# Kernel optimization log

Measured on AMD Instinct MI355X. Metric: run time of the kernel, lower is better.

## Reference

```python
import jax, jax.numpy as jnp
import numpy as np

# Inner model dims (concrete MLP standing in for the wrapped keras model)
D_IN, HID, D_OUT = 1024, 2048, 10
POP, STD = 40, 0.1
S1 = D_IN * HID          # end of W1
S2 = S1 + HID            # end of b1
S3 = S2 + HID * D_OUT    # end of W2
N_PARAMS = S3 + D_OUT    # 2,119,690


def _flatten_weights(W1, b1, W2, b2):
    # tf.concat([reshape(w, [-1]) for w in trainable_weights])
    return jnp.concatenate([W1.reshape(-1), b1, W2.reshape(-1), b2])


def _mse_loss(flat_w, x, y):
    # expand_flat_trainable_weights + forward + compiled_loss (MSE)
    W1 = flat_w[:S1].reshape(D_IN, HID)
    b1 = flat_w[S1:S2]
    W2 = flat_w[S2:S3].reshape(HID, D_OUT)
    b2 = flat_w[S3:]
    pred = jax.nn.relu(x @ W1 + b1) @ W2 + b2
    return jnp.mean((pred - y) ** 2)


def _centered_ranks(t):
    # compute_centered_ranks: argsort-based ranks in [0, n), centered to [-0.5, 0.5]
    flat = t.reshape(-1)
    n = flat.shape[0]
    ranks = jnp.zeros((n,), jnp.float32).at[jnp.argsort(flat)].set(
        jnp.arange(n, dtype=jnp.float32))
    return (ranks / (n - 1) - 0.5).reshape(t.shape)


def setup_inputs() -> dict:
    key = jax.random.key(0)
    ks = jax.random.split(key, 5)
    return {
        "x": jax.random.normal(ks[0], (256, D_IN), jnp.float32),
        "y": jax.random.normal(ks[1], (256, D_OUT), jnp.float32),
        "W1": jax.random.normal(ks[2], (D_IN, HID), jnp.float32) * 0.02,
        "b1": jnp.zeros((HID,), jnp.float32),
        "W2": jax.random.normal(ks[3], (HID, D_OUT), jnp.float32) * 0.02,
        "b2": jnp.zeros((D_OUT,), jnp.float32),
        "noise": jax.random.normal(ks[4], (POP, N_PARAMS), jnp.float32),
    }


def reference(x, y, W1, b1, W2, b2, noise):
    flat_w = _flatten_weights(W1, b1, W2, b2)          # [N]
    eps = noise * STD                                   # stddev-scaled noise [POP, N]
    # parity: i even -> +1, i odd -> -1 (antithetic pairs)
    parity = jnp.array([1.0, -1.0], jnp.float32)
    perturbed = flat_w[None, None, :] + eps[:, None, :] * parity[None, :, None]  # [POP,2,N]
    # batched replacement for the pop_size*2 sequential forward passes
    losses = jax.vmap(jax.vmap(lambda w: _mse_loss(w, x, y)))(perturbed)  # [POP, 2]
    proc = _centered_ranks(losses)
    proc = proc[:, 0] - proc[:, 1]                      # [POP]
    grad = jnp.tensordot(eps, proc, axes=[[0], [0]]) / (POP * STD)  # [N]
    return grad
```

## Files before the change

### kernel.cpp

```cpp
#include <hip/hip_runtime.h>


#define NPLL 2119690LL
#define S1_  2097152
#define S2_  2099200
#define S3_  2119680

#define WS_PP   524288
#define WS_LOSS 3801088
#define WS_G    3801168

typedef _Float16 f16;
typedef __fp16   fp16x2 __attribute__((ext_vector_type(2)));
typedef _Float16 f16x8 __attribute__((ext_vector_type(8)));
typedef float    f32x4 __attribute__((ext_vector_type(4)));

__device__ __forceinline__ unsigned pk2r(float a, float b, float& ra, float& rb) {
  fp16x2 h = __builtin_amdgcn_cvt_pkrtz(a, b);
  ra = a - (float)h[0];
  rb = b - (float)h[1];
  return __builtin_bit_cast(unsigned, h);
}
__device__ __forceinline__ unsigned pk2(float a, float b) {
  fp16x2 h = __builtin_amdgcn_cvt_pkrtz(a, b);
  return __builtin_bit_cast(unsigned, h);
}

__global__ __launch_bounds__(256) void k_base(const float* __restrict__ x,
                                              const float* __restrict__ W1,
                                              const float* __restrict__ b1,
                                              float* __restrict__ base) {
  constexpr int STR = 72;
  __shared__ float xs[32 * STR];
  __shared__ float es[32 * STR];
  const int t  = threadIdx.x;
  const int j0 = blockIdx.x * 64;
  const int b0 = blockIdx.y * 32;
  const int tj = t & 15;
  const int tb = t >> 4;
  float acc[4][2] = {};
  for (int k0 = 0; k0 < 1024; k0 += 32) {
    __syncthreads();
    {
      int bb = t >> 3, kq = t & 7;
      float4 v = *(const float4*)&x[(size_t)(b0 + bb) * 1024 + k0 + kq * 4];
      int kb = kq * 4;
      xs[(kb + 0) * STR + bb] = v.x;
      xs[(kb + 1) * STR + bb] = v.y;
      xs[(kb + 2) * STR + bb] = v.z;
      xs[(kb + 3) * STR + bb] = v.w;
    }
#pragma unroll
    for (int r = 0; r < 2; ++r) {
      int idx = t + r * 256;
      int k = idx >> 4, jq = idx & 15, col = jq * 4;
      float4 v = *(const float4*)&W1[(size_t)(k0 + k) * 2048 + j0 + col];
      *(float4*)&es[k * STR + col + 4 * (col >> 5)] = v;
    }
    __syncthreads();
#pragma unroll 8
    for (int k = 0; k < 32; ++k) {
      const int ce = tj * 4;
      float4 e = *(const float4*)&es[k * STR + ce + 4 * (ce >> 5)];
      float2 a = *(const float2*)&xs[k * STR + tb * 2];
      acc[0][0] += e.x * a.x; acc[0][1] += e.x * a.y;
      acc[1][0] += e.y * a.x; acc[1][1] += e.y * a.y;
      acc[2][0] += e.z * a.x; acc[2][1] += e.z * a.y;
      acc[3][0] += e.w * a.x; acc[3][1] += e.w * a.y;
    }
  }
#pragma unroll
  for (int jj = 0; jj < 4; ++jj) {
    int j = j0 + tj * 4 + jj;
    float bv = b1[j];
    float2 o = make_float2(acc[jj][0] + bv, acc[jj][1] + bv);
    *(float2*)&base[(size_t)j * 256 + b0 + tb * 2] = o;
  }
}

#define ESTR 72
__global__ __launch_bounds__(256, 2) void k_big(const float* __restrict__ x,
                                                const float* __restrict__ noise,
                                                const float* __restrict__ W2,
                                                const float* __restrict__ base,
                                                float* __restrict__ pp) {
  __shared__ __align__(16) f16 eA[128 * ESTR];
  __shared__ __align__(16) f16 xB[128 * ESTR];
  __shared__ float w2l[1280], e2l[1280], e1l[128];
  __shared__ float red[1280];

  const int t    = threadIdx.x;
  const int p    = blockIdx.x >> 1, bt = blockIdx.x & 1, jt = blockIdx.y;
  const int j0   = jt * 128, b0 = bt * 128;
  const int wave = t >> 6, lane = t & 63;
  const int lm   = lane & 15, g8 = (lane >> 4) * 8;
  const int g4   = (lane >> 4) * 4;
  const int wj0  = (wave & 1) * 64, wb0 = (wave >> 1) * 64;
  const size_t pN = (size_t)p * NPLL;
  const int rl = t & 63;
  const int kq = (t >> 6) * 8;

  for (int i = t; i < 1280; i += 256) {
    w2l[i] = W2[j0 * 10 + i];
    e2l[i] = noise[pN + S2_ + (size_t)j0 * 10 + i];
  }
  if (t < 128) e1l[t] = noise[pN + S1_ + j0 + t];

  float vE0[8], vE1[8], vX0[8], vX1[8];
  f32x4 acc[4][4];
#pragma unroll
  for (int a = 0; a < 4; ++a)
#pragma unroll
    for (int b = 0; b < 4; ++b) acc[a][b] = (f32x4){0.f, 0.f, 0.f, 0.f};

#define LOADK(K0)                                                              \
  do {                                                                         \
    const float* eg = &noise[pN + (size_t)((K0) + kq) * 2048 + j0 + rl];       \
    _Pragma("unroll") for (int d = 0; d < 8; ++d) {                            \
      vE0[d] = eg[(size_t)d * 2048];                                           \
      vE1[d] = eg[(size_t)d * 2048 + 64];                                      \
    }                                                                          \
    const float* xg = &x[(size_t)(b0 + rl) * 1024 + (K0) + kq];                \
    float4 a0 = *(const float4*)xg;                                            \
    float4 a1 = *(const float4*)(xg + 4);                                      \
    float4 c0 = *(const float4*)(xg + 65536);                                  \
    float4 c1 = *(const float4*)(xg + 65540);                                  \
    vX0[0] = a0.x; vX0[1] = a0.y; vX0[2] = a0.z; vX0[3] = a0.w;                \
    vX0[4] = a1.x; vX0[5] = a1.y; vX0[6] = a1.z; vX0[7] = a1.w;                \
    vX1[0] = c0.x; vX1[1] = c0.y; vX1[2] = c0.z; vX1[3] = c0.w;                \
    vX1[4] = c1.x; vX1[5] = c1.y; vX1[6] = c1.z; vX1[7] = c1.w;                \
  } while (0)

#define CVW(V, DST)                                                            \
  do {                                                                         \
    float r0, r1, r2, r3, r4, r5, r6, r7;                                      \
    uint4 H, L;                                                                \
    H.x = pk2r(V[0], V[1], r0, r1);                                            \
    H.y = pk2r(V[2], V[3], r2, r3);                                            \
    H.z = pk2r(V[4], V[5], r4, r5);                                            \
    H.w = pk2r(V[6], V[7], r6, r7);                                            \
    *(uint4*)(DST) = H;                                                        \
    L.x = pk2(r0, r1); L.y = pk2(r2, r3);                                      \
    L.z = pk2(r4, r5); L.w = pk2(r6, r7);                                      \
    *(uint4*)((DST) + 32) = L;                                                 \
  } while (0)

  LOADK(0);
  for (int ks = 0; ks < 32; ++ks) {
    __syncthreads();
    CVW(vE0, &eA[rl * ESTR + kq]);
    CVW(vE1, &eA[(rl + 64) * ESTR + kq]);
    CVW(vX0, &xB[rl * ESTR + kq]);
    CVW(vX1, &xB[(rl + 64) * ESTR + kq]);
    if (ks < 31) LOADK((ks + 1) * 32);
    __syncthreads();
    f16x8 Ah[4], Al[4], Bh[4], Bl[4];
#pragma unroll
    for (int mf = 0; mf < 4; ++mf) {
      Ah[mf] = *(const f16x8*)&eA[(wj0 + mf * 16 + lm) * ESTR + g8];
      Al[mf] = *(const f16x8*)&eA[(wj0 + mf * 16 + lm) * ESTR + 32 + g8];
      Bh[mf] = *(const f16x8*)&xB[(wb0 + mf * 16 + lm) * ESTR + g8];
      Bl[mf] = *(const f16x8*)&xB[(wb0 + mf * 16 + lm) * ESTR + 32 + g8];
    }
#pragma unroll
    for (int mf = 0; mf < 4; ++mf)
#pragma unroll
      for (int nf = 0; nf < 4; ++nf) {
        acc[mf][nf] = __builtin_amdgcn_mfma_f32_16x16x32_f16(Ah[mf], Bh[nf], acc[mf][nf], 0, 0, 0);
        acc[mf][nf] = __builtin_amdgcn_mfma_f32_16x16x32_f16(Ah[mf], Bl[nf], acc[mf][nf], 0, 0, 0);
        acc[mf][nf] = __builtin_amdgcn_mfma_f32_16x16x32_f16(Al[mf], Bh[nf], acc[mf][nf], 0, 0, 0);
      }
  }

  float ppvP[4][10] = {};
  float ppvM[4][10] = {};
#pragma unroll
  for (int mf = 0; mf < 4; ++mf)
#pragma unroll
    for (int r = 0; r < 4; ++r) {
      const int jl = wj0 + mf * 16 + g4 + r;
      const float e1v = e1l[jl];
      float w2p[10], w2m[10];
#pragma unroll
      for (int o = 0; o < 10; ++o) {
        float w2 = w2l[jl * 10 + o], e2 = e2l[jl * 10 + o];
        w2p[o] = fmaf(0.1f, e2, w2);
        w2m[o] = fmaf(-0.1f, e2, w2);
      }
#pragma unroll
      for (int nf = 0; nf < 4; ++nf) {
        const int bl = wb0 + nf * 16 + lm;
        const float bs = base[(size_t)(j0 + jl) * 256 + b0 + bl];
        const float tv = acc[mf][nf][r] + e1v;
        const float hp = fmaxf(fmaf(0.1f, tv, bs), 0.f);
        const float hm = fmaxf(fmaf(-0.1f, tv, bs), 0.f);
#pragma unroll
        for (int o = 0; o < 10; ++o) {
          ppvP[nf][o] = fmaf(hp, w2p[o], ppvP[nf][o]);
          ppvM[nf][o] = fmaf(hm, w2m[o], ppvM[nf][o]);
        }
      }
    }

#pragma unroll
  for (int nf = 0; nf < 4; ++nf)
#pragma unroll
    for (int o = 0; o < 10; ++o) {
      float v = ppvP[nf][o];
      v += __shfl_xor(v, 16, 64);
      v += __shfl_xor(v, 32, 64);
      ppvP[nf][o] = v;
      float u = ppvM[nf][o];
      u += __shfl_xor(u, 16, 64);
      u += __shfl_xor(u, 32, 64);
      ppvM[nf][o] = u;
    }

  const int wjh = wave & 1, wbh = wave >> 1;
  __syncthreads();
  if (wjh == 1 && lane < 16) {
#pragma unroll
    for (int nf = 0; nf < 4; ++nf)
#pragma unroll
      for (int o = 0; o < 10; ++o)
        red[(wbh * 64 + nf * 16 + lane) * 10 + o] = ppvP[nf][o];
  }
  __syncthreads();
  if (wjh == 0 && lane < 16) {
#pragma unroll
    for (int nf = 0; nf < 4; ++nf) {
      const int bl = wbh * 64 + nf * 16 + lane;
#pragma unroll
      for (int o = 0; o < 10; ++o)
        pp[((((size_t)p * 2 + 0) * 16 + jt) * 256 + b0 + bl) * 10 + o] =
            ppvP[nf][o] + red[bl * 10 + o];
    }
  }
  __syncthreads();
  if (wjh == 1 && lane < 16) {
#pragma unroll
    for (int nf = 0; nf < 4; ++nf)
#pragma unroll
      for (int o = 0; o < 10; ++o)
        red[(wbh * 64 + nf * 16 + lane) * 10 + o] = ppvM[nf][o];
  }
  __syncthreads();
  if (wjh == 0 && lane < 16) {
#pragma unroll
    for (int nf = 0; nf < 4; ++nf) {
      const int bl = wbh * 64 + nf * 16 + lane;
#pragma unroll
      for (int o = 0; o < 10; ++o)
        pp[((((size_t)p * 2 + 1) * 16 + jt) * 256 + b0 + bl) * 10 + o] =
            ppvM[nf][o] + red[bl * 10 + o];
    }
  }
#undef LOADK
#undef CVW
}

__global__ __launch_bounds__(256) void k_loss(const float* __restrict__ pp,
                                              const float* __restrict__ y,
                                              const float* __restrict__ b2,
                                              const float* __restrict__ noise,
                                              float* __restrict__ loss) {
  const int b = threadIdx.x;
  const int p = blockIdx.x >> 1, s = blockIdx.x & 1;
  const float sf = s ? -0.1f : 0.1f;
  const size_t pN = (size_t)p * NPLL;
  float pred[10];
#pragma unroll
  for (int o = 0; o < 10; ++o) pred[o] = b2[o] + sf * noise[pN + S3_ + o];
  for (int jt = 0; jt < 16; ++jt) {
    const float* src = &pp[((((size_t)p * 2 + s) * 16 + jt) * 256 + b) * 10];
#pragma unroll
    for (int o = 0; o < 10; ++o) pred[o] += src[o];
  }
  float e = 0.f;
#pragma unroll
  for (int o = 0; o < 10; ++o) {
    float d = pred[o] - y[b * 10 + o];
    e += d * d;
  }
  __shared__ float red[256];
  red[b] = e;
  __syncthreads();
  for (int st = 128; st > 0; st >>= 1) {
    if (b < st) red[b] += red[b + st];
    __syncthreads();
  }
  if (b == 0) loss[blockIdx.x] = red[0] * (1.0f / 2560.0f);
}

__global__ void k_rank(const float* __restrict__ loss, float* __restrict__ g) {
  __shared__ float ls[80];
  __shared__ float rk[80];
  const int t = threadIdx.x;
  if (t < 80) ls[t] = loss[t];
  __syncthreads();
  if (t < 80) {
    float li = ls[t];
    int r = 0;
    for (int j = 0; j < 80; ++j) {
      float lj = ls[j];
      r += (lj < li) || (lj == li && j < t);
    }
    rk[t] = (float)r;
  }
  __syncthreads();
  if (t < 40) g[t] = (rk[2 * t] - rk[2 * t + 1]) * (1.0f / (79.0f * 40.0f));
}

__global__ __launch_bounds__(256) void k_grad(const float* __restrict__ noise,
                                              const float* __restrict__ g,
                                              float* __restrict__ out) {
  __shared__ float gg[40];
  const int t = threadIdx.x;
  if (t < 40) gg[t] = g[t];
  __syncthreads();
  const long long NH = NPLL / 2;
  long long idx = (long long)blockIdx.x * 256 + t;
  if (idx >= NH) return;
  float2 a = make_float2(0.f, 0.f);
#pragma unroll 8
  for (int p = 0; p < 40; ++p) {
    float2 v = *(const float2*)&noise[(size_t)p * NPLL + idx * 2];
    a.x += v.x * gg[p];
    a.y += v.y * gg[p];
  }
  *(float2*)&out[idx * 2] = a;
}

extern "C" void kernel_launch(void* const* d_in, const int* in_sizes, int n_in,
                              void* d_out, int out_size, void* d_ws, size_t ws_size,
                              hipStream_t stream) {
  const float* x     = (const float*)d_in[0];
  const float* y     = (const float*)d_in[1];
  const float* W1    = (const float*)d_in[2];
  const float* b1    = (const float*)d_in[3];
  const float* W2    = (const float*)d_in[4];
  const float* b2    = (const float*)d_in[5];
  const float* noise = (const float*)d_in[6];
  float* out  = (float*)d_out;
  float* ws   = (float*)d_ws;
  float* base = ws;
  float* pp   = ws + WS_PP;
  float* loss = ws + WS_LOSS;
  float* g    = ws + WS_G;

  k_base<<<dim3(32, 8), 256, 0, stream>>>(x, W1, b1, base);
  k_big<<<dim3(80, 16), 256, 0, stream>>>(x, noise, W2, base, pp);
  k_loss<<<80, 256, 0, stream>>>(pp, y, b2, noise, loss);
  k_rank<<<1, 128, 0, stream>>>(loss, g);
  k_grad<<<4141, 256, 0, stream>>>(noise, g, out);
}
```

Before: 390.7 us.

## Retile big kernel over full batch, presplit x to fp16 hi/lo, store fp16 partials

Each k_big block now covers 64 hidden units across all 256 batch rows instead of 128x128, so each noise element is loaded once rather than twice. A new kernel splits x into fp16 hi/lo halves up front, and k_big reads those directly from global memory, dropping the per-block conversion and the LDS staging of x. The epilogue loops over the two signs to cut register pressure. Per-tile partial predictions are stored as packed fp16, which lowers traffic but adds rounding error to the losses and could change their ranking.

```diff
diff --git a/kernel.cpp b/kernel.cpp
--- a/kernel.cpp
+++ b/kernel.cpp
@@ -9,6 +9,8 @@
 #define WS_PP   524288
 #define WS_LOSS 3801088
 #define WS_G    3801168
+#define WS_XH   3801216
+#define WS_XL   3932288
 
 typedef _Float16 f16;
 typedef __fp16   fp16x2 __attribute__((ext_vector_type(2)));
@@ -24,6 +26,11 @@
 __device__ __forceinline__ unsigned pk2(float a, float b) {
   fp16x2 h = __builtin_amdgcn_cvt_pkrtz(a, b);
   return __builtin_bit_cast(unsigned, h);
+}
+__device__ __forceinline__ unsigned packh(float a, float b) {
+  union { f16 h[2]; unsigned u; } v;
+  v.h[0] = (f16)a; v.h[1] = (f16)b;
+  return v.u;
 }
 
 __global__ __launch_bounds__(256) void k_base(const float* __restrict__ x,
@@ -78,89 +85,94 @@
   }
 }
 
+__global__ __launch_bounds__(256) void k_xsplit(const float* __restrict__ x,
+                                                f16* __restrict__ xh,
+                                                f16* __restrict__ xl) {
+  const int i = (blockIdx.x * 256 + threadIdx.x) * 8;
+  float4 a = *(const float4*)&x[i];
+  float4 b = *(const float4*)&x[i + 4];
+  float v[8] = {a.x, a.y, a.z, a.w, b.x, b.y, b.z, b.w};
+  float r[8];
+  uint4 H, L;
+  H.x = pk2r(v[0], v[1], r[0], r[1]);
+  H.y = pk2r(v[2], v[3], r[2], r[3]);
+  H.z = pk2r(v[4], v[5], r[4], r[5]);
+  H.w = pk2r(v[6], v[7], r[6], r[7]);
+  L.x = pk2(r[0], r[1]); L.y = pk2(r[2], r[3]);
+  L.z = pk2(r[4], r[5]); L.w = pk2(r[6], r[7]);
+  *(uint4*)&xh[i] = H;
+  *(uint4*)&xl[i] = L;
+}
+
 #define ESTR 72
-__global__ __launch_bounds__(256, 2) void k_big(const float* __restrict__ x,
+__global__ __launch_bounds__(256, 2) void k_big(const f16* __restrict__ xh,
+                                                const f16* __restrict__ xl,
                                                 const float* __restrict__ noise,
                                                 const float* __restrict__ W2,
                                                 const float* __restrict__ base,
-                                                float* __restrict__ pp) {
-  __shared__ __align__(16) f16 eA[128 * ESTR];
-  __shared__ __align__(16) f16 xB[128 * ESTR];
-  __shared__ float w2l[1280], e2l[1280], e1l[128];
-  __shared__ float red[1280];
+                                                unsigned* __restrict__ ppu) {
+  __shared__ __align__(16) f16 eA[64 * ESTR];
+  __shared__ float w2l[640], e2l[640], e1l[64];
 
   const int t    = threadIdx.x;
-  const int p    = blockIdx.x >> 1, bt = blockIdx.x & 1, jt = blockIdx.y;
-  const int j0   = jt * 128, b0 = bt * 128;
+  const int jt   = blockIdx.x, p = blockIdx.y;
+  const int j0   = jt * 64;
   const int wave = t >> 6, lane = t & 63;
-  const int lm   = lane & 15, g8 = (lane >> 4) * 8;
-  const int g4   = (lane >> 4) * 4;
-  const int wj0  = (wave & 1) * 64, wb0 = (wave >> 1) * 64;
+  const int lm   = lane & 15, g8 = (lane >> 4) * 8, g4 = (lane >> 4) * 4;
+  const int wb   = wave;
   const size_t pN = (size_t)p * NPLL;
-  const int rl = t & 63;
-  const int kq = (t >> 6) * 8;
-
-  for (int i = t; i < 1280; i += 256) {
+  const int rl = lane;
+  const int kq = wave * 8;
+
+  for (int i = t; i < 640; i += 256) {
     w2l[i] = W2[j0 * 10 + i];
     e2l[i] = noise[pN + S2_ + (size_t)j0 * 10 + i];
   }
-  if (t < 128) e1l[t] = noise[pN + S1_ + j0 + t];
-
-  float vE0[8], vE1[8], vX0[8], vX1[8];
+  if (t < 64) e1l[t] = noise[pN + S1_ + j0 + t];
+
+  float ve[8];
   f32x4 acc[4][4];
 #pragma unroll
   for (int a = 0; a < 4; ++a)
 #pragma unroll
     for (int b = 0; b < 4; ++b) acc[a][b] = (f32x4){0.f, 0.f, 0.f, 0.f};
 
-#define LOADK(K0)                                                              \
+#define LOADE(K0)                                                              \
   do {                                                                         \
     const float* eg = &noise[pN + (size_t)((K0) + kq) * 2048 + j0 + rl];       \
-    _Pragma("unroll") for (int d = 0; d < 8; ++d) {                            \
-      vE0[d] = eg[(size_t)d * 2048];                                           \
-      vE1[d] = eg[(size_t)d * 2048 + 64];                                      \
-    }                                                                          \
-    const float* xg = &x[(size_t)(b0 + rl) * 1024 + (K0) + kq];                \
-    float4 a0 = *(const float4*)xg;                                            \
-    float4 a1 = *(const float4*)(xg + 4);                                      \
-    float4 c0 = *(const float4*)(xg + 65536);                                  \
-    float4 c1 = *(const float4*)(xg + 65540);                                  \
-    vX0[0] = a0.x; vX0[1] = a0.y; vX0[2] = a0.z; vX0[3] = a0.w;                \
-    vX0[4] = a1.x; vX0[5] = a1.y; vX0[6] = a1.z; vX0[7] = a1.w;                \
-    vX1[0] = c0.x; vX1[1] = c0.y; vX1[2] = c0.z; vX1[3] = c0.w;                \
-    vX1[4] = c1.x; vX1[5] = c1.y; vX1[6] = c1.z; vX1[7] = c1.w;                \
+    _Pragma("unroll") for (int d = 0; d < 8; ++d) ve[d] = eg[(size_t)d * 2048];\
   } while (0)
 
-#define CVW(V, DST)                                                            \
-  do {                                                                         \
-    float r0, r1, r2, r3, r4, r5, r6, r7;                                      \
-    uint4 H, L;                                                                \
-    H.x = pk2r(V[0], V[1], r0, r1);                                            \
-    H.y = pk2r(V[2], V[3], r2, r3);                                            \
-    H.z = pk2r(V[4], V[5], r4, r5);                                            \
-    H.w = pk2r(V[6], V[7], r6, r7);                                            \
-    *(uint4*)(DST) = H;                                                        \
-    L.x = pk2(r0, r1); L.y = pk2(r2, r3);                                      \
-    L.z = pk2(r4, r5); L.w = pk2(r6, r7);                                      \
-    *(uint4*)((DST) + 32) = L;                                                 \
-  } while (0)
-
-  LOADK(0);
+  LOADE(0);
   for (int ks = 0; ks < 32; ++ks) {
-    __syncthreads();
-    CVW(vE0, &eA[rl * ESTR + kq]);
-    CVW(vE1, &eA[(rl + 64) * ESTR + kq]);
-    CVW(vX0, &xB[rl * ESTR + kq]);
-    CVW(vX1, &xB[(rl + 64) * ESTR + kq]);
-    if (ks < 31) LOADK((ks + 1) * 32);
-    __syncthreads();
-    f16x8 Ah[4], Al[4], Bh[4], Bl[4];
+    const int k0 = ks * 32;
+    __syncthreads();
+    {
+      float r0, r1, r2, r3, r4, r5, r6, r7;
+      uint4 H, L;
+      H.x = pk2r(ve[0], ve[1], r0, r1);
+      H.y = pk2r(ve[2], ve[3], r2, r3);
+      H.z = pk2r(ve[4], ve[5], r4, r5);
+      H.w = pk2r(ve[6], ve[7], r6, r7);
+      *(uint4*)&eA[rl * ESTR + kq] = H;
+      L.x = pk2(r0, r1); L.y = pk2(r2, r3);
+      L.z = pk2(r4, r5); L.w = pk2(r6, r7);
+      *(uint4*)&eA[rl * ESTR + 32 + kq] = L;
+    }
+    f16x8 Bh[4], Bl[4];
+#pragma unroll
+    for (int nf = 0; nf < 4; ++nf) {
+      const size_t bo = (size_t)(wb * 64 + nf * 16 + lm) * 1024 + k0 + g8;
+      Bh[nf] = *(const f16x8*)&xh[bo];
+      Bl[nf] = *(const f16x8*)&xl[bo];
+    }
+    if (ks < 31) LOADE((ks + 1) * 32);
+    __syncthreads();
+    f16x8 Ah[4], Al[4];
 #pragma unroll
     for (int mf = 0; mf < 4; ++mf) {
-      Ah[mf] = *(const f16x8*)&eA[(wj0 + mf * 16 + lm) * ESTR + g8];
-      Al[mf] = *(const f16x8*)&eA[(wj0 + mf * 16 + lm) * ESTR + 32 + g8];
-      Bh[mf] = *(const f16x8*)&xB[(wb0 + mf * 16 + lm) * ESTR + g8];
-      Bl[mf] = *(const f16x8*)&xB[(wb0 + mf * 16 + lm) * ESTR + 32 + g8];
+      Ah[mf] = *(const f16x8*)&eA[(mf * 16 + lm) * ESTR + g8];
+      Al[mf] = *(const f16x8*)&eA[(mf * 16 + lm) * ESTR + 32 + g8];
     }
 #pragma unroll
     for (int mf = 0; mf < 4; ++mf)
@@ -172,94 +184,59 @@
       }
   }
 
-  float ppvP[4][10] = {};
-  float ppvM[4][10] = {};
-#pragma unroll
-  for (int mf = 0; mf < 4; ++mf)
-#pragma unroll
-    for (int r = 0; r < 4; ++r) {
-      const int jl = wj0 + mf * 16 + g4 + r;
-      const float e1v = e1l[jl];
-      float w2p[10], w2m[10];
-#pragma unroll
-      for (int o = 0; o < 10; ++o) {
-        float w2 = w2l[jl * 10 + o], e2 = e2l[jl * 10 + o];
-        w2p[o] = fmaf(0.1f, e2, w2);
-        w2m[o] = fmaf(-0.1f, e2, w2);
-      }
-#pragma unroll
-      for (int nf = 0; nf < 4; ++nf) {
-        const int bl = wb0 + nf * 16 + lm;
-        const float bs = base[(size_t)(j0 + jl) * 256 + b0 + bl];
-        const float tv = acc[mf][nf][r] + e1v;
-        const float hp = fmaxf(fmaf(0.1f, tv, bs), 0.f);
-        const float hm = fmaxf(fmaf(-0.1f, tv, bs), 0.f);
-#pragma unroll
-        for (int o = 0; o < 10; ++o) {
-          ppvP[nf][o] = fmaf(hp, w2p[o], ppvP[nf][o]);
-          ppvM[nf][o] = fmaf(hm, w2m[o], ppvM[nf][o]);
+#pragma unroll 1
+  for (int s = 0; s < 2; ++s) {
+    const float sf = s ? -0.1f : 0.1f;
+    float ppv[4][10];
+#pragma unroll
+    for (int nf = 0; nf < 4; ++nf)
+#pragma unroll
+      for (int o = 0; o < 10; ++o) ppv[nf][o] = 0.f;
+#pragma unroll
+    for (int mf = 0; mf < 4; ++mf)
+#pragma unroll
+      for (int r = 0; r < 4; ++r) {
+        const int jl = mf * 16 + g4 + r;
+        const float e1v = e1l[jl];
+        float w2s[10];
+#pragma unroll
+        for (int o = 0; o < 10; ++o)
+          w2s[o] = fmaf(sf, e2l[jl * 10 + o], w2l[jl * 10 + o]);
+#pragma unroll
+        for (int nf = 0; nf < 4; ++nf) {
+          const int bl = wb * 64 + nf * 16 + lm;
+          const float bs = base[(size_t)(j0 + jl) * 256 + bl];
+          const float h = fmaxf(fmaf(sf, acc[mf][nf][r] + e1v, bs), 0.f);
+#pragma unroll
+          for (int o = 0; o < 10; ++o) ppv[nf][o] = fmaf(h, w2s[o], ppv[nf][o]);
         }
       }
-    }
-
-#pragma unroll
-  for (int nf = 0; nf < 4; ++nf)
-#pragma unroll
-    for (int o = 0; o < 10; ++o) {
-      float v = ppvP[nf][o];
-      v += __shfl_xor(v, 16, 64);
-      v += __shfl_xor(v, 32, 64);
-      ppvP[nf][o] = v;
-      float u = ppvM[nf][o];
-      u += __shfl_xor(u, 16, 64);
-      u += __shfl_xor(u, 32, 64);
-      ppvM[nf][o] = u;
-    }
-
-  const int wjh = wave & 1, wbh = wave >> 1;
-  __syncthreads();
-  if (wjh == 1 && lane < 16) {
 #pragma unroll
     for (int nf = 0; nf < 4; ++nf)
 #pragma unroll
-      for (int o = 0; o < 10; ++o)
-        red[(wbh * 64 + nf * 16 + lane) * 10 + o] = ppvP[nf][o];
-  }
-  __syncthreads();
-  if (wjh == 0 && lane < 16) {
-#pragma unroll
-    for (int nf = 0; nf < 4; ++nf) {
-      const int bl = wbh * 64 + nf * 16 + lane;
-#pragma unroll
-      for (int o = 0; o < 10; ++o)
-        pp[((((size_t)p * 2 + 0) * 16 + jt) * 256 + b0 + bl) * 10 + o] =
-            ppvP[nf][o] + red[bl * 10 + o];
-    }
-  }
-  __syncthreads();
-  if (wjh == 1 && lane < 16) {
-#pragma unroll
-    for (int nf = 0; nf < 4; ++nf)
-#pragma unroll
-      for (int o = 0; o < 10; ++o)
-        red[(wbh * 64 + nf * 16 + lane) * 10 + o] = ppvM[nf][o];
-  }
-  __syncthreads();
-  if (wjh == 0 && lane < 16) {
-#pragma unroll
-    for (int nf = 0; nf < 4; ++nf) {
-      const int bl = wbh * 64 + nf * 16 + lane;
-#pragma unroll
-      for (int o = 0; o < 10; ++o)
-        pp[((((size_t)p * 2 + 1) * 16 + jt) * 256 + b0 + bl) * 10 + o] =
-            ppvM[nf][o] + red[bl * 10 + o];
-    }
-  }
-#undef LOADK
-#undef CVW
-}
-
-__global__ __launch_bounds__(256) void k_loss(const float* __restrict__ pp,
+      for (int o = 0; o < 10; ++o) {
+        float v = ppv[nf][o];
+        v += __shfl_xor(v, 16, 64);
+        v += __shfl_xor(v, 32, 64);
+        ppv[nf][o] = v;
+      }
+    if (lane < 16) {
+#pragma unroll
+      for (int nf = 0; nf < 4; ++nf) {
+        const int bl = wb * 64 + nf * 16 + lm;
+        const size_t u0 = ((((size_t)p * 2 + s) * 32 + jt) * 256 + bl) * 5;
+        ppu[u0 + 0] = packh(ppv[nf][0], ppv[nf][1]);
+        ppu[u0 + 1] = packh(ppv[nf][2], ppv[nf][3]);
+        ppu[u0 + 2] = packh(ppv[nf][4], ppv[nf][5]);
+        ppu[u0 + 3] = packh(ppv[nf][6], ppv[nf][7]);
+        ppu[u0 + 4] = packh(ppv[nf][8], ppv[nf][9]);
+      }
+    }
+  }
+#undef LOADE
+}
+
+__global__ __launch_bounds__(256) void k_loss(const unsigned* __restrict__ ppu,
                                               const float* __restrict__ y,
                                               const float* __restrict__ b2,
                                               const float* __restrict__ noise,
@@ -271,10 +248,15 @@
   float pred[10];
 #pragma unroll
   for (int o = 0; o < 10; ++o) pred[o] = b2[o] + sf * noise[pN + S3_ + o];
-  for (int jt = 0; jt < 16; ++jt) {
-    const float* src = &pp[((((size_t)p * 2 + s) * 16 + jt) * 256 + b) * 10];
-#pragma unroll
-    for (int o = 0; o < 10; ++o) pred[o] += src[o];
+  for (int jt = 0; jt < 32; ++jt) {
+    const size_t u0 = ((((size_t)p * 2 + s) * 32 + jt) * 256 + b) * 5;
+#pragma unroll
+    for (int q = 0; q < 5; ++q) {
+      union { unsigned u; f16 h[2]; } w;
+      w.u = ppu[u0 + q];
+      pred[2 * q]     += (float)w.h[0];
+      pred[2 * q + 1] += (float)w.h[1];
+    }
   }
   float e = 0.f;
 #pragma unroll
@@ -344,13 +326,16 @@
   float* out  = (float*)d_out;
   float* ws   = (float*)d_ws;
   float* base = ws;
-  float* pp   = ws + WS_PP;
+  unsigned* ppu = (unsigned*)(ws + WS_PP);
   float* loss = ws + WS_LOSS;
   float* g    = ws + WS_G;
+  f16* xh = (f16*)(ws + WS_XH);
+  f16* xl = (f16*)(ws + WS_XL);
 
   k_base<<<dim3(32, 8), 256, 0, stream>>>(x, W1, b1, base);
-  k_big<<<dim3(80, 16), 256, 0, stream>>>(x, noise, W2, base, pp);
-  k_loss<<<80, 256, 0, stream>>>(pp, y, b2, noise, loss);
+  k_xsplit<<<128, 256, 0, stream>>>(x, xh, xl);
+  k_big<<<dim3(32, 40), 256, 0, stream>>>(xh, xl, noise, W2, base, ppu);
+  k_loss<<<80, 256, 0, stream>>>(ppu, y, b2, noise, loss);
   k_rank<<<1, 128, 0, stream>>>(loss, g);
   k_grad<<<4141, 256, 0, stream>>>(noise, g, out);
 }
```

After: 594.9 us. +52.3%, slower.
